# Kernel optimization log

Measured on AMD Instinct MI355X. Metric: run time of the kernel, lower is better.

Reference implementation:

```python
import jax, jax.numpy as jnp
import numpy as np
from jax import lax

CAP_UNITS = 49
CAP_SIZE = 8

def setup_inputs() -> dict:
    key = jax.random.key(0)
    k1, k2, k3 = jax.random.split(key, 3)
    x = jax.random.normal(k1, (128, 16, 64, 64), dtype=jnp.float32)
    # 49 ConvUnits (16->8, 9x9) stacked into one conv weight [49*8, 16, 9, 9]
    fan_in = 16 * 9 * 9
    bound = 1.0 / np.sqrt(fan_in)
    W = jax.random.uniform(k2, (CAP_UNITS * CAP_SIZE, 16, 9, 9), jnp.float32, -bound, bound)
    b = jax.random.uniform(k3, (CAP_UNITS * CAP_SIZE,), jnp.float32, -bound, bound)
    return {"x": x, "W": W, "b": b}

def squash(s, axis):
    mag_sq = jnp.sum(s * s, axis=axis, keepdims=True)
    mag = jnp.sqrt(mag_sq)
    return mag_sq / (1.0 + mag_sq) * (s / mag)

def reference(x, W, b):
    B = x.shape[0]
    # single fused conv == 49 parallel 16->8 convs, 9x9, stride 2, VALID
    h = lax.conv_general_dilated(
        x, W, window_strides=(2, 2), padding='VALID',
        dimension_numbers=('NCHW', 'OIHW', 'NCHW'))
    h = h + b[None, :, None, None]                    # [B, 49*8, H', W']
    Hp, Wp = h.shape[2], h.shape[3]
    u = h.reshape(B, CAP_UNITS, CAP_SIZE, Hp * Wp)    # [B, 49, 8, HW]
    # torch ordering: cat over units on dim 3 -> [B,8,HW,49] -> flatten -> capsule idx = hw*49 + unit
    u = u.transpose(0, 3, 1, 2).reshape(B, Hp * Wp * CAP_UNITS, CAP_SIZE)
    return squash(u, axis=2)
```

## Files before the change

### kernel.cpp

```cpp
#include <hip/hip_runtime.h>


typedef __attribute__((ext_vector_type(8)))  short short8;
typedef __attribute__((ext_vector_type(16))) float f32x16;

constexpr int Bn = 128, Units = 49, Cap = 8, OW = 28, HWp = 784;
constexpr int Nn = 392, Npad = 448;
constexpr int BM = 512, BNt = 64, NB = 7;
constexpr int NKS = 41;
constexpr size_t XW_BYTES = (size_t)Bn * 64 * 64 * 16 * 2;
constexpr size_t BW_BYTES = (size_t)NKS * 4 * Npad * 8 * 2;

__device__ inline unsigned short f2bf(float f) {
    unsigned u = __float_as_uint(f);
    u += 0x7FFF + ((u >> 16) & 1);
    return (unsigned short)(u >> 16);
}

__device__ __forceinline__ void gload16(const void* g, void* l) {
    __builtin_amdgcn_global_load_lds(
        (const __attribute__((address_space(1))) unsigned int*)g,
        (__attribute__((address_space(3))) unsigned int*)l, 16, 0, 0);
}

__global__ __launch_bounds__(256) void prep_x(const float* __restrict__ x,
                                              unsigned short* __restrict__ xw) {
    __shared__ unsigned short tile[64 * 16];
    const int b = blockIdx.x >> 6, y = blockIdx.x & 63;
    const int t = threadIdx.x;
    const int c = t >> 4, x0 = (t & 15) * 4;
    const float4 v = *(const float4*)(x + (((size_t)b * 16 + c) * 64 + y) * 64 + x0);
    tile[(x0 + 0) * 16 + c] = f2bf(v.x);
    tile[(x0 + 1) * 16 + c] = f2bf(v.y);
    tile[(x0 + 2) * 16 + c] = f2bf(v.z);
    tile[(x0 + 3) * 16 + c] = f2bf(v.w);
    __syncthreads();
    const ushort4 o = *(const ushort4*)&tile[t * 4];
    *(ushort4*)(xw + (size_t)blockIdx.x * 1024 + t * 4) = o;
}

__global__ __launch_bounds__(256) void prep_w(const float* __restrict__ W,
                                              unsigned short* __restrict__ bw) {
    const int idx = blockIdx.x * 256 + threadIdx.x;
    if (idx >= NKS * 4 * Npad) return;
    const int n    = idx % Npad;
    const int rest = idx / Npad;
    const int h = rest & 1, tt = (rest >> 1) & 1, ks = rest >> 2;
    const int p = ks * 2 + tt;
    unsigned short vals[8];
    if (p < 81 && n < Nn) {
#pragma unroll
        for (int j = 0; j < 8; ++j)
            vals[j] = f2bf(W[(size_t)(n * 16 + h * 8 + j) * 81 + p]);
    } else {
#pragma unroll
        for (int j = 0; j < 8; ++j) vals[j] = 0;
    }
    *(ushort4*)(bw + (size_t)idx * 8)     = make_ushort4(vals[0], vals[1], vals[2], vals[3]);
    *(ushort4*)(bw + (size_t)idx * 8 + 4) = make_ushort4(vals[4], vals[5], vals[6], vals[7]);
}

#define MFMA32(A, B, C) __builtin_amdgcn_mfma_f32_32x32x16_bf16(A, B, C, 0, 0, 0)

constexpr int ABUF = 32768;
constexpr int LBUF = ABUF + 4096;

__global__ __launch_bounds__(256, 2) void pcaps_lds(
    const unsigned short* __restrict__ xw,
    const unsigned short* __restrict__ bw,
    const float* __restrict__ bias,
    float* __restrict__ out)
{
    __shared__ __align__(16) char lds[2][LBUF];

    const int t = threadIdx.x;
    const int nwg = gridDim.x;
    const int q8 = nwg >> 3, r8 = nwg & 7;
    const int xcd = blockIdx.x & 7, idx8 = blockIdx.x >> 3;
    const int wgid = (xcd < r8 ? xcd * (q8 + 1) : r8 * (q8 + 1) + (xcd - r8) * q8) + idx8;
    const int nb = wgid % NB, mb = wgid / NB;
    const int n0 = nb * BNt;

    const int w = t >> 6, l = t & 63;
    const int r = l & 31, h = l >> 5;

    int arow_off[8];
    int asel[8];
#pragma unroll
    for (int it = 0; it < 8; ++it) {
        const int q = t + 256 * it;
        const int row = q >> 2;
        const int piece = (q & 3) ^ ((row >> 1) & 3);
        const int tq = piece >> 1, hq = piece & 1;
        const int m = mb * BM + row;
        const int b = m / HWp;
        const int hw = m - b * HWp;
        const int oy = hw / OW, ox = hw - oy * OW;
        arow_off[it] = b * 131072 + oy * 4096 + ox * 64 + hq * 16;
        asel[it] = tq;
    }
    const int bglob0 = (w * Npad + n0 + l) * 16;
    constexpr int bstep = 4 * Npad * 16;

    int aoff[4][2];
#pragma unroll
    for (int mi = 0; mi < 4; ++mi) {
        const int row = w * 128 + mi * 32 + r;
        const int cid0 = (row * 4 + h) ^ ((row >> 1) & 3);
        aoff[mi][0] = cid0 * 16;
        aoff[mi][1] = (cid0 ^ 2) * 16;
    }
    int boff[2][2];
#pragma unroll
    for (int ni = 0; ni < 2; ++ni)
#pragma unroll
        for (int tt = 0; tt < 2; ++tt)
            boff[ni][tt] = ABUF + ((tt * 2 + h) * 64 + ni * 32 + r) * 16;

    f32x16 acc[4][2];
#pragma unroll
    for (int mi = 0; mi < 4; ++mi)
#pragma unroll
        for (int ni = 0; ni < 2; ++ni)
#pragma unroll
            for (int e = 0; e < 16; ++e) acc[mi][ni][e] = 0.f;

    const char* __restrict__ xcc = (const char*)xw;
    const char* __restrict__ bcc = (const char*)bw;

    auto stage = [&](char* base, int o0, int o1, int bks) {
#pragma unroll
        for (int it = 0; it < 8; ++it)
            gload16(xcc + (arow_off[it] + (asel[it] ? o1 : o0)),
                    base + (t + 256 * it) * 16);
        gload16(bcc + (bglob0 + bks), base + ABUF + t * 16);
    };

    stage(lds[0], 0, 32, 0);
    __syncthreads();

    int ky = 0, kx = 2;
    int cur = 0;
    for (int ks = 0; ks < NKS; ++ks) {
        if (ks + 1 < NKS) {
            const int o0 = ky * 2048 + kx * 32;
            int kx1 = kx + 1, ky1 = ky;
            if (kx1 == 9) { kx1 = 0; ky1 += 1; }
            const int o1 = ky1 * 2048 + kx1 * 32;
            stage(lds[cur ^ 1], o0, o1, (ks + 1) * bstep);
            kx += 2; if (kx >= 9) { kx -= 9; ky += 1; }
        }

        const char* base = lds[cur];
        short8 afr[4][2], bfr[2][2];
#pragma unroll
        for (int mi = 0; mi < 4; ++mi)
#pragma unroll
            for (int tt = 0; tt < 2; ++tt)
                afr[mi][tt] = *(const short8*)(base + aoff[mi][tt]);
#pragma unroll
        for (int ni = 0; ni < 2; ++ni)
#pragma unroll
            for (int tt = 0; tt < 2; ++tt)
                bfr[ni][tt] = *(const short8*)(base + boff[ni][tt]);

#pragma unroll
        for (int tt = 0; tt < 2; ++tt)
#pragma unroll
            for (int mi = 0; mi < 4; ++mi)
#pragma unroll
                for (int ni = 0; ni < 2; ++ni)
                    acc[mi][ni] = MFMA32(afr[mi][tt], bfr[ni][tt], acc[mi][ni]);

        __syncthreads();
        cur ^= 1;
    }

    float bv[2];
#pragma unroll
    for (int ni = 0; ni < 2; ++ni) {
        const int n = n0 + ni * 32 + r;
        bv[ni] = (n < Nn) ? bias[n] : 0.f;
    }
#pragma unroll
    for (int mi = 0; mi < 4; ++mi) {
#pragma unroll
        for (int ni = 0; ni < 2; ++ni) {
            const int n = n0 + ni * 32 + r;
            const bool nok = (n < Nn);
#pragma unroll
            for (int reg = 0; reg < 16; ++reg) {
                float e = acc[mi][ni][reg] + bv[ni];
                float sq = e * e;
                sq += __shfl_xor(sq, 1);
                sq += __shfl_xor(sq, 2);
                sq += __shfl_xor(sq, 4);
                const float scale = sqrtf(sq) / (1.0f + sq);
                if (nok) {
                    const int rowc = (reg & 3) + 8 * (reg >> 2) + 4 * h;
                    const int m = mb * BM + w * 128 + mi * 32 + rowc;
                    out[(size_t)m * Nn + n] = e * scale;
                }
            }
        }
    }
}

__global__ __launch_bounds__(128) void pcaps_direct(
    const float* __restrict__ x, const float* __restrict__ W,
    const float* __restrict__ bias, float* __restrict__ out)
{
    const int blk = blockIdx.x;
    const int tile = blk % 7;
    const int u = (blk / 7) % Units;
    const int b = blk / (7 * Units);
    const int hw = tile * 128 + threadIdx.x;
    const bool active = (hw < HWp);
    const int oy = active ? (hw / OW) : 0;
    const int ox = active ? (hw % OW) : 0;
    const float* xb = x + (size_t)b * (16 * 64 * 64) + (size_t)(oy * 2) * 64 + ox * 2;
    const float* wu = W + (size_t)u * (Cap * 1296);
    float acc[Cap];
#pragma unroll
    for (int j = 0; j < Cap; ++j) acc[j] = bias[u * Cap + j];
    for (int c = 0; c < 16; ++c) {
        const float* xcp = xb + c * (64 * 64);
        const float* wc = wu + c * 81;
#pragma unroll
        for (int ky = 0; ky < 9; ++ky) {
            const float* xr = xcp + ky * 64;
            float xv[9];
#pragma unroll
            for (int kx = 0; kx < 9; ++kx) xv[kx] = xr[kx];
#pragma unroll
            for (int kx = 0; kx < 9; ++kx)
#pragma unroll
                for (int j = 0; j < Cap; ++j)
                    acc[j] = fmaf(xv[kx], wc[j * 1296 + ky * 9 + kx], acc[j]);
        }
    }
    if (active) {
        float msq = 0.f;
#pragma unroll
        for (int j = 0; j < Cap; ++j) msq = fmaf(acc[j], acc[j], msq);
        const float scale = sqrtf(msq) / (1.0f + msq);
        float* op = out + (size_t)b * (HWp * Nn) + (size_t)hw * Nn + u * Cap;
        float4 o0, o1;
        o0.x = acc[0] * scale; o0.y = acc[1] * scale; o0.z = acc[2] * scale; o0.w = acc[3] * scale;
        o1.x = acc[4] * scale; o1.y = acc[5] * scale; o1.z = acc[6] * scale; o1.w = acc[7] * scale;
        *reinterpret_cast<float4*>(op) = o0;
        *reinterpret_cast<float4*>(op + 4) = o1;
    }
}

extern "C" void kernel_launch(void* const* d_in, const int* in_sizes, int n_in,
                              void* d_out, int out_size, void* d_ws, size_t ws_size,
                              hipStream_t stream)
{
    const float* x  = (const float*)d_in[0];
    const float* W  = (const float*)d_in[1];
    const float* bs = (const float*)d_in[2];
    float* out      = (float*)d_out;

    if (ws_size < XW_BYTES + BW_BYTES) {
        pcaps_direct<<<Bn * Units * 7, 128, 0, stream>>>(x, W, bs, out);
        return;
    }

    unsigned short* xw = (unsigned short*)d_ws;
    unsigned short* bw = (unsigned short*)((char*)d_ws + XW_BYTES);

    prep_x<<<Bn * 64, 256, 0, stream>>>(x, xw);
    prep_w<<<(NKS * 4 * Npad + 255) / 256, 256, 0, stream>>>(W, bw);
    pcaps_lds<<<(100352 / BM) * NB, 256, 0, stream>>>(xw, bw, bs, out);
}
```

Baseline: 220.7 us.

## Split LDS staging around MFMA halves with fine-grained vmcnt waits and setprio

The main K loop now splits the next-stage global-to-LDS copies into two batches: 5 A loads before the first MFMA half and the remaining A loads plus the B load between the two MFMA halves. A partial `s_waitcnt vmcnt(5)` plus a raw barrier replaces the full `__syncthreads` drain, so only the current buffer's loads must have landed before reading it. MFMA sections are wrapped in `s_setprio` and the last K step is peeled into an epilogue. The aim is to keep more global loads in flight during compute, at the cost of relying on exact counting of outstanding loads for correctness.

```diff
diff --git a/kernel.cpp b/kernel.cpp
--- a/kernel.cpp
+++ b/kernel.cpp
@@ -61,6 +61,8 @@
 }
 
 #define MFMA32(A, B, C) __builtin_amdgcn_mfma_f32_32x32x16_bf16(A, B, C, 0, 0, 0)
+#define SBAR() do { __builtin_amdgcn_s_barrier(); \
+                    __builtin_amdgcn_sched_barrier(0); } while (0)
 
 constexpr int ABUF = 32768;
 constexpr int LBUF = ABUF + 4096;
@@ -128,52 +130,86 @@
     const char* __restrict__ xcc = (const char*)xw;
     const char* __restrict__ bcc = (const char*)bw;
 
-    auto stage = [&](char* base, int o0, int o1, int bks) {
+    auto stageA = [&](char* basep, int o0, int o1, int lo, int hi) {
 #pragma unroll
         for (int it = 0; it < 8; ++it)
-            gload16(xcc + (arow_off[it] + (asel[it] ? o1 : o0)),
-                    base + (t + 256 * it) * 16);
-        gload16(bcc + (bglob0 + bks), base + ABUF + t * 16);
+            if (it >= lo && it < hi)
+                gload16(xcc + (arow_off[it] + (asel[it] ? o1 : o0)),
+                        basep + (t + 256 * it) * 16);
     };
 
-    stage(lds[0], 0, 32, 0);
-    __syncthreads();
+    stageA(lds[0], 0, 32, 0, 8);
+    gload16(bcc + bglob0, lds[0] + ABUF + t * 16);
 
     int ky = 0, kx = 2;
     int cur = 0;
-    for (int ks = 0; ks < NKS; ++ks) {
-        if (ks + 1 < NKS) {
-            const int o0 = ky * 2048 + kx * 32;
-            int kx1 = kx + 1, ky1 = ky;
-            if (kx1 == 9) { kx1 = 0; ky1 += 1; }
-            const int o1 = ky1 * 2048 + kx1 * 32;
-            stage(lds[cur ^ 1], o0, o1, (ks + 1) * bstep);
-            kx += 2; if (kx >= 9) { kx -= 9; ky += 1; }
+    for (int ks = 0; ks < NKS - 1; ++ks) {
+        const int o0 = ky * 2048 + kx * 32;
+        int kx1 = kx + 1, ky1 = ky;
+        if (kx1 == 9) { kx1 = 0; ky1 += 1; }
+        const int o1 = ky1 * 2048 + kx1 * 32;
+        kx += 2; if (kx >= 9) { kx -= 9; ky += 1; }
+
+        char* nbuf = lds[cur ^ 1];
+        const char* base = lds[cur];
+
+        stageA(nbuf, o0, o1, 0, 5);
+        asm volatile("s_waitcnt vmcnt(5)" ::: "memory");
+        SBAR();
+
+        short8 afr0[4], bfr0[2];
+#pragma unroll
+        for (int mi = 0; mi < 4; ++mi) afr0[mi] = *(const short8*)(base + aoff[mi][0]);
+        bfr0[0] = *(const short8*)(base + boff[0][0]);
+        bfr0[1] = *(const short8*)(base + boff[1][0]);
+
+        __builtin_amdgcn_s_setprio(1);
+#pragma unroll
+        for (int mi = 0; mi < 4; ++mi)
+#pragma unroll
+            for (int ni = 0; ni < 2; ++ni)
+                acc[mi][ni] = MFMA32(afr0[mi], bfr0[ni], acc[mi][ni]);
+        __builtin_amdgcn_s_setprio(0);
+        __builtin_amdgcn_sched_barrier(0);
+
+        stageA(nbuf, o0, o1, 5, 8);
+        gload16(bcc + (bglob0 + (ks + 1) * bstep), nbuf + ABUF + t * 16);
+
+        short8 afr1[4], bfr1[2];
+#pragma unroll
+        for (int mi = 0; mi < 4; ++mi) afr1[mi] = *(const short8*)(base + aoff[mi][1]);
+        bfr1[0] = *(const short8*)(base + boff[0][1]);
+        bfr1[1] = *(const short8*)(base + boff[1][1]);
+
+        __builtin_amdgcn_s_setprio(1);
+#pragma unroll
+        for (int mi = 0; mi < 4; ++mi)
+#pragma unroll
+            for (int ni = 0; ni < 2; ++ni)
+                acc[mi][ni] = MFMA32(afr1[mi], bfr1[ni], acc[mi][ni]);
+        __builtin_amdgcn_s_setprio(0);
+
+        SBAR();
+        cur ^= 1;
+    }
+
+    asm volatile("s_waitcnt vmcnt(0)" ::: "memory");
+    SBAR();
+    {
+        const char* base = lds[cur];
+#pragma unroll
+        for (int tt = 0; tt < 2; ++tt) {
+            short8 afr[4], bfr[2];
+#pragma unroll
+            for (int mi = 0; mi < 4; ++mi) afr[mi] = *(const short8*)(base + aoff[mi][tt]);
+            bfr[0] = *(const short8*)(base + boff[0][tt]);
+            bfr[1] = *(const short8*)(base + boff[1][tt]);
+#pragma unroll
+            for (int mi = 0; mi < 4; ++mi)
+#pragma unroll
+                for (int ni = 0; ni < 2; ++ni)
+                    acc[mi][ni] = MFMA32(afr[mi], bfr[ni], acc[mi][ni]);
         }
-
-        const char* base = lds[cur];
-        short8 afr[4][2], bfr[2][2];
-#pragma unroll
-        for (int mi = 0; mi < 4; ++mi)
-#pragma unroll
-            for (int tt = 0; tt < 2; ++tt)
-                afr[mi][tt] = *(const short8*)(base + aoff[mi][tt]);
-#pragma unroll
-        for (int ni = 0; ni < 2; ++ni)
-#pragma unroll
-            for (int tt = 0; tt < 2; ++tt)
-                bfr[ni][tt] = *(const short8*)(base + boff[ni][tt]);
-
-#pragma unroll
-        for (int tt = 0; tt < 2; ++tt)
-#pragma unroll
-            for (int mi = 0; mi < 4; ++mi)
-#pragma unroll
-                for (int ni = 0; ni < 2; ++ni)
-                    acc[mi][ni] = MFMA32(afr[mi][tt], bfr[ni][tt], acc[mi][ni]);
-
-        __syncthreads();
-        cur ^= 1;
     }
 
     float bv[2];
```

Measured after the change: 226.6 us. 1.03x slower.
